# Kernel tuning notes

Hardware: AMD Instinct MI355X
Metric: run time of the kernel (lower is better)

The kernel has to match this reference:

```python
import jax, jax.numpy as jnp
import numpy as np

B, T, H = 2, 2048, 1024
NH = 16
HD = H // NH


def setup_inputs() -> dict:
    key = jax.random.key(0)
    ks = jax.random.split(key, 9)
    s = 0.02
    return {
        "x": jax.random.normal(ks[0], (B, T, H), dtype=jnp.float32),
        "attn_mask": jnp.ones((B, T), dtype=jnp.int32),
        "Wq": jax.random.normal(ks[1], (H, H), dtype=jnp.float32) * s,
        "bq": jnp.zeros((H,), dtype=jnp.float32),
        "Wk": jax.random.normal(ks[2], (H, H), dtype=jnp.float32) * s,
        "bk": jnp.zeros((H,), dtype=jnp.float32),
        "Wv": jax.random.normal(ks[3], (H, H), dtype=jnp.float32) * s,
        "bv": jnp.zeros((H,), dtype=jnp.float32),
        "Wo": jax.random.normal(ks[4], (H, H), dtype=jnp.float32) * s,
        "bo": jnp.zeros((H,), dtype=jnp.float32),
    }


def reference(x, attn_mask, Wq, bq, Wk, bk, Wv, bv, Wo, bo):
    Bc, Tc, Hc = x.shape
    scale = HD ** -0.5
    # projections; torch Linear: y = x @ W.T + b (here W stored as [in,out])
    q = (x @ Wq + bq).reshape(Bc, Tc, NH, HD).transpose(0, 2, 1, 3)  # [B,NH,T,HD]
    k = (x @ Wk + bk).reshape(Bc, Tc, NH, HD).transpose(0, 2, 1, 3)
    v = (x @ Wv + bv).reshape(Bc, Tc, NH, HD).transpose(0, 2, 1, 3)
    scores = jnp.einsum('bhqd,bhkd->bhqk', q, k) * scale  # [B,NH,T,T]
    mask = attn_mask.reshape(Bc, 1, 1, Tc)
    scores = jnp.where(mask == 0, jnp.float32(-jnp.inf), scores)
    probs = jax.nn.softmax(scores, axis=-1)
    ctx = jnp.einsum('bhqk,bhkd->bhqd', probs, v)  # [B,NH,T,HD]
    ctx = ctx.transpose(0, 2, 1, 3).reshape(Bc, Tc, Hc)
    out = ctx @ Wo + bo
    return out
```

## Files before the change

### kernel.cpp

```cpp
#include <hip/hip_runtime.h>

typedef _Float16 f16;
typedef _Float16 f16x8 __attribute__((ext_vector_type(8)));
typedef _Float16 f16x4 __attribute__((ext_vector_type(4)));
typedef __fp16 h16x2 __attribute__((ext_vector_type(2)));
typedef float f32x4 __attribute__((ext_vector_type(4)));

#define MFMA32(a, b, c) __builtin_amdgcn_mfma_f32_16x16x32_f16((a), (b), (c), 0, 0, 0)

static constexpr int Bb = 2, T = 2048, H = 1024, NH = 16, HD = 64;
static constexpr int M = Bb * T;
static constexpr int NQK = 2 * H;
#define QSCALE 0.1803368801111f

__device__ __forceinline__ void gload_lds16(const void* g, void* l) {
  __builtin_amdgcn_global_load_lds(
      (const __attribute__((address_space(1))) void*)g,
      (__attribute__((address_space(3))) void*)l, 16, 0, 0);
}

__global__ __launch_bounds__(256) void pack_all(const float* __restrict__ x,
                                                const float* __restrict__ Wq,
                                                const float* __restrict__ Wk,
                                                const float* __restrict__ Wv,
                                                const float* __restrict__ Wo,
                                                const float* __restrict__ bq,
                                                const float* __restrict__ bk,
                                                const float* __restrict__ bv,
                                                const int* __restrict__ mask,
                                                f16* __restrict__ xh,
                                                f16* __restrict__ WqkvT,
                                                f16* __restrict__ WoT,
                                                float* __restrict__ bqkv,
                                                float* __restrict__ maskf) {
  __shared__ f16 tile[64][65];
  const int bid = blockIdx.x;
  if (bid < 4096) {
    int i = bid * 256 + threadIdx.x;
    float4 v = ((const float4*)x)[i];
    f16x4 o;
    o[0] = (f16)v.x; o[1] = (f16)v.y; o[2] = (f16)v.z; o[3] = (f16)v.w;
    *(f16x4*)(xh + (size_t)i * 4) = o;
  } else if (bid < 5120) {
    int t = bid - 4096;
    int z = t >> 8, rem = t & 255;
    const float* W = (z == 0) ? Wq : (z == 1) ? Wk : (z == 2) ? Wv : Wo;
    f16* Wt = (z < 3) ? (WqkvT + (size_t)z * H * H) : WoT;
    const float scale = (z == 0) ? QSCALE : 1.0f;
    int k0 = (rem >> 4) * 64, n0 = (rem & 15) * 64;
    for (int p = 0; p < 16; ++p) {
      int idx = threadIdx.x + p * 256;
      int r = idx >> 6, c = idx & 63;
      tile[r][c] = (f16)(W[(size_t)(k0 + r) * H + n0 + c] * scale);
    }
    __syncthreads();
    for (int p = 0; p < 16; ++p) {
      int idx = threadIdx.x + p * 256;
      int r = idx >> 6, c = idx & 63;
      Wt[(size_t)(n0 + r) * H + k0 + c] = tile[c][r];
    }
  } else if (bid < 5132) {
    int i = (bid - 5120) * 256 + threadIdx.x;
    if (i < 3072) {
      float v = (i < 1024) ? bq[i] * QSCALE : ((i < 2048) ? bk[i - 1024] : bv[i - 2048]);
      bqkv[i] = v;
    }
  } else {
    int i = (bid - 5132) * 256 + threadIdx.x;
    if (i < Bb * T) maskf[i] = mask[i] ? 0.0f : -30000.0f;
  }
}

__device__ __forceinline__ f16x8 lds_frag(const f16* base, int row, int gr) {
  return *(const f16x8*)(base + row * 64 + ((gr ^ (row & 7)) << 3));
}

__global__ __launch_bounds__(256, 3) void gemm_qkv(const f16* __restrict__ A,
                                                   const f16* __restrict__ Bt,
                                                   const float* __restrict__ bias,
                                                   f16* __restrict__ QK,
                                                   f16* __restrict__ VT) {
  constexpr int TM = 128, TN = 64, Kk = 1024;
  __shared__ f16 As[2][TM * 64];
  __shared__ f16 Bs[2][TN * 64];
  const int tid = threadIdx.x;
  const int lane = tid & 63, w = tid >> 6;
  const int quad = lane >> 4, l16 = lane & 15;
  const int wm = w >> 1, wn = w & 1;
  const int m0 = blockIdx.y * TM, n0 = blockIdx.x * TN;

  f32x4 acc[4][2];
  for (int a = 0; a < 4; ++a)
    for (int b2 = 0; b2 < 2; ++b2)
      for (int r = 0; r < 4; ++r) acc[a][b2][r] = 0.f;

  auto stage = [&](int k0, int buf) {
    for (int p = 0; p < 4; ++p) {
      int slot = p * 256 + w * 64 + lane;
      int r = slot >> 3, g = (slot & 7) ^ (r & 7);
      gload_lds16(A + (size_t)(m0 + r) * Kk + k0 + g * 8,
                  (char*)&As[buf][0] + (p * 256 + w * 64) * 16);
    }
    for (int p = 0; p < 2; ++p) {
      int slot = p * 256 + w * 64 + lane;
      int r = slot >> 3, g = (slot & 7) ^ (r & 7);
      gload_lds16(Bt + (size_t)(n0 + r) * Kk + k0 + g * 8,
                  (char*)&Bs[buf][0] + (p * 256 + w * 64) * 16);
    }
  };

  stage(0, 0);
  __syncthreads();
  for (int it = 0; it < Kk / 64; ++it) {
    const int cur = it & 1;
    if (it + 1 < Kk / 64) stage((it + 1) * 64, cur ^ 1);
    for (int ks = 0; ks < 2; ++ks) {
      f16x8 af[4], bf[2];
      for (int t = 0; t < 4; ++t)
        af[t] = lds_frag(&As[cur][0], wm * 64 + t * 16 + l16, ks * 4 + quad);
      for (int t = 0; t < 2; ++t)
        bf[t] = lds_frag(&Bs[cur][0], wn * 32 + t * 16 + l16, ks * 4 + quad);
      for (int tm = 0; tm < 4; ++tm)
        for (int tn = 0; tn < 2; ++tn)
          acc[tm][tn] = MFMA32(af[tm], bf[tn], acc[tm][tn]);
    }
    __syncthreads();
  }

  if (n0 < 2048) {
    for (int tm = 0; tm < 4; ++tm)
      for (int tn = 0; tn < 2; ++tn) {
        int n = n0 + wn * 32 + tn * 16 + l16;
        float bn = bias[n];
        for (int r = 0; r < 4; ++r) {
          int m = m0 + wm * 64 + tm * 16 + quad * 4 + r;
          QK[(size_t)m * NQK + n] = (f16)(acc[tm][tn][r] + bn);
        }
      }
  } else {
    for (int tm = 0; tm < 4; ++tm)
      for (int tn = 0; tn < 2; ++tn) {
        int ng = n0 + wn * 32 + tn * 16 + l16;
        float bn = bias[ng];
        int n = ng - 2048;
        int h = n >> 6, d = n & 63;
        int mrow = m0 + wm * 64 + tm * 16 + quad * 4;
        int bb = mrow >> 11, t = mrow & 2047;
        int c = (t & ~127) | ((t + 8 * (d & 15)) & 127);
        f16x4 o;
        for (int r = 0; r < 4; ++r) o[r] = (f16)(acc[tm][tn][r] + bn);
        *(f16x4*)(VT + ((size_t)(bb * NH + h) * HD + d) * T + c) = o;
      }
  }
}

__global__ __launch_bounds__(256, 3) void gemm_out(const f16* __restrict__ A,
                                                   const f16* __restrict__ Bt,
                                                   const float* __restrict__ bias,
                                                   float* __restrict__ Cout) {
  constexpr int TM = 128, TN = 64, Kk = 1024, Nn = 1024;
  __shared__ f16 As[2][TM * 64];
  __shared__ f16 Bs[2][TN * 64];
  const int tid = threadIdx.x;
  const int lane = tid & 63, w = tid >> 6;
  const int quad = lane >> 4, l16 = lane & 15;
  const int wm = w >> 1, wn = w & 1;
  const int m0 = blockIdx.y * TM, n0 = blockIdx.x * TN;

  f32x4 acc[4][2];
  for (int a = 0; a < 4; ++a)
    for (int b2 = 0; b2 < 2; ++b2)
      for (int r = 0; r < 4; ++r) acc[a][b2][r] = 0.f;

  auto stage = [&](int k0, int buf) {
    for (int p = 0; p < 4; ++p) {
      int slot = p * 256 + w * 64 + lane;
      int r = slot >> 3, g = (slot & 7) ^ (r & 7);
      gload_lds16(A + (size_t)(m0 + r) * Kk + k0 + g * 8,
                  (char*)&As[buf][0] + (p * 256 + w * 64) * 16);
    }
    for (int p = 0; p < 2; ++p) {
      int slot = p * 256 + w * 64 + lane;
      int r = slot >> 3, g = (slot & 7) ^ (r & 7);
      gload_lds16(Bt + (size_t)(n0 + r) * Kk + k0 + g * 8,
                  (char*)&Bs[buf][0] + (p * 256 + w * 64) * 16);
    }
  };

  stage(0, 0);
  __syncthreads();
  for (int it = 0; it < Kk / 64; ++it) {
    const int cur = it & 1;
    if (it + 1 < Kk / 64) stage((it + 1) * 64, cur ^ 1);
    for (int ks = 0; ks < 2; ++ks) {
      f16x8 af[4], bf[2];
      for (int t = 0; t < 4; ++t)
        af[t] = lds_frag(&As[cur][0], wm * 64 + t * 16 + l16, ks * 4 + quad);
      for (int t = 0; t < 2; ++t)
        bf[t] = lds_frag(&Bs[cur][0], wn * 32 + t * 16 + l16, ks * 4 + quad);
      for (int tm = 0; tm < 4; ++tm)
        for (int tn = 0; tn < 2; ++tn)
          acc[tm][tn] = MFMA32(af[tm], bf[tn], acc[tm][tn]);
    }
    __syncthreads();
  }

  for (int tm = 0; tm < 4; ++tm)
    for (int tn = 0; tn < 2; ++tn) {
      int n = n0 + wn * 32 + tn * 16 + l16;
      float bn = bias[n];
      for (int r = 0; r < 4; ++r) {
        int m = m0 + wm * 64 + tm * 16 + quad * 4 + r;
        Cout[(size_t)m * Nn + n] = acc[tm][tn][r] + bn;
      }
    }
}


static constexpr int KT_ELE = 128 * 64;
static constexpr int VT_ELE = 64 * 128;

__global__ __launch_bounds__(512, 2) void attn_fused(const f16* __restrict__ QK,
                                                     const f16* __restrict__ VT,
                                                     const float* __restrict__ maskf,
                                                     f16* __restrict__ ctx) {
  __shared__ __align__(16) char smem[70656];
  f16* KtB = (f16*)smem;
  f16* VtB = (f16*)(smem + 2 * KT_ELE * 2);

  const int tid = threadIdx.x;
  const int w = tid >> 6, lane = tid & 63;
  const int quad = lane >> 4, l16 = lane & 15;
  const int qw = w & 3, g = w >> 2;

  const int flat = blockIdx.x + (T / 256) * (blockIdx.y + NH * blockIdx.z);
  const int xcd = flat & 7, idx = flat >> 3;
  const int bh = xcd * 4 + (idx >> 3);
  const int qb = idx & 7;
  const int h = bh & 15, b = bh >> 4;
  const int q0 = qb * 256;

  const size_t kbase = (size_t)(b * T) * NQK + H + h * HD;
  const size_t vtbase = ((size_t)(b * NH + h) * HD) * T;
  const float* maskp = maskf + b * T;

  f16x8 qf[4][2];
  for (int tq = 0; tq < 4; ++tq) {
    const f16* qrow = QK + (size_t)(b * T + q0 + qw * 64 + tq * 16 + l16) * NQK + h * HD;
    qf[tq][0] = *(const f16x8*)(qrow + quad * 8);
    qf[tq][1] = *(const f16x8*)(qrow + 32 + quad * 8);
  }

  f16x8 onesf;
  for (int i = 0; i < 8; ++i) onesf[i] = (f16)1.0f;

  f32x4 oacc[4][4];
  f32x4 lacc[4];
  for (int tq = 0; tq < 4; ++tq) {
    for (int r = 0; r < 4; ++r) lacc[tq][r] = 0.f;
    for (int t = 0; t < 4; ++t)
      for (int r = 0; r < 4; ++r) oacc[tq][t][r] = 0.f;
  }

  auto stage = [&](int kv0, int buf) {
    f16* Kd = KtB + buf * KT_ELE;
    f16* Vd = VtB + buf * VT_ELE;
    for (int p = 0; p < 2; ++p) {
      int s = p * 512 + tid;
      int R = s >> 3, sg = (s & 7) ^ (R & 7);
      int kv = (R & ~31) | ((R & 12) << 1) | ((R & 16) >> 2) | (R & 3);
      gload_lds16(QK + kbase + (size_t)(kv0 + kv) * NQK + sg * 8,
                  (char*)Kd + (p * 512 + w * 64) * 16);
    }
    for (int p = 0; p < 2; ++p) {
      int s = p * 512 + tid;
      int d = s >> 4, cg = s & 15;
      gload_lds16(VT + vtbase + (size_t)d * T + kv0 + cg * 8,
                  (char*)Vd + (p * 512 + w * 64) * 16);
    }
  };

  stage(0, 0);
  __syncthreads();

  for (int it = 0; it < T / 128; ++it) {
    const int cur = it & 1;
    if (it + 1 < T / 128) stage((it + 1) * 128, cur ^ 1);

    const f16* Kc = KtB + cur * KT_ELE;
    const f16* Vc = VtB + cur * VT_ELE;

    for (int s = 0; s < 2; ++s) {
      const int bi = g * 2 + s;
      const int kvabs = it * 128 + bi * 32;
      float4 m0 = *(const float4*)(maskp + kvabs + quad * 8);
      float4 m1 = *(const float4*)(maskp + kvabs + quad * 8 + 4);
      f32x4 zA, zB;
      zA[0] = m0.x; zA[1] = m0.y; zA[2] = m0.z; zA[3] = m0.w;
      zB[0] = m1.x; zB[1] = m1.y; zB[2] = m1.z; zB[3] = m1.w;
      f16x8 kfA0 = lds_frag(Kc, bi * 32 + l16, quad);
      f16x8 kfA1 = lds_frag(Kc, bi * 32 + l16, 4 + quad);
      f16x8 kfB0 = lds_frag(Kc, bi * 32 + 16 + l16, quad);
      f16x8 kfB1 = lds_frag(Kc, bi * 32 + 16 + l16, 4 + quad);
      f16x8 vf[4];
      for (int td = 0; td < 4; ++td)
        vf[td] = *(const f16x8*)&Vc[(td * 16 + l16) * 128 +
                                    ((bi * 32 + quad * 8 + 8 * l16) & 127)];

      f32x4 sA[4], sB[4];
      for (int tq = 0; tq < 4; ++tq) {
        sA[tq] = MFMA32(kfA0, qf[tq][0], zA);
        sB[tq] = MFMA32(kfB0, qf[tq][0], zB);
      }
      for (int tq = 0; tq < 4; ++tq) {
        sA[tq] = MFMA32(kfA1, qf[tq][1], sA[tq]);
        sB[tq] = MFMA32(kfB1, qf[tq][1], sB[tq]);
      }

      f16x8 pf[4];
      for (int tq = 0; tq < 4; ++tq) {
        float pA0 = __builtin_amdgcn_exp2f(sA[tq][0]);
        float pA1 = __builtin_amdgcn_exp2f(sA[tq][1]);
        float pA2 = __builtin_amdgcn_exp2f(sA[tq][2]);
        float pA3 = __builtin_amdgcn_exp2f(sA[tq][3]);
        float pB0 = __builtin_amdgcn_exp2f(sB[tq][0]);
        float pB1 = __builtin_amdgcn_exp2f(sB[tq][1]);
        float pB2 = __builtin_amdgcn_exp2f(sB[tq][2]);
        float pB3 = __builtin_amdgcn_exp2f(sB[tq][3]);
        union PF { f16x8 v; h16x2 h[4]; } u;
        u.h[0] = __builtin_amdgcn_cvt_pkrtz(pA0, pA1);
        u.h[1] = __builtin_amdgcn_cvt_pkrtz(pA2, pA3);
        u.h[2] = __builtin_amdgcn_cvt_pkrtz(pB0, pB1);
        u.h[3] = __builtin_amdgcn_cvt_pkrtz(pB2, pB3);
        pf[tq] = u.v;
      }

      for (int tq = 0; tq < 4; ++tq) {
        for (int td = 0; td < 4; ++td)
          oacc[tq][td] = MFMA32(vf[td], pf[tq], oacc[tq][td]);
        lacc[tq] = MFMA32(onesf, pf[tq], lacc[tq]);
      }
    }
    __syncthreads();
  }

  float* cmb = (float*)smem;
  const int slot = qw * 64 + lane;
  if (g == 1) {
    float* dst = cmb + slot * 69;
    int i = 0;
    for (int tq = 0; tq < 4; ++tq)
      for (int td = 0; td < 4; ++td)
        for (int r = 0; r < 4; ++r) dst[i++] = oacc[tq][td][r];
    for (int tq = 0; tq < 4; ++tq) dst[64 + tq] = lacc[tq][0];
  }
  __syncthreads();
  if (g == 0) {
    const float* src = cmb + slot * 69;
    int i = 0;
    for (int tq = 0; tq < 4; ++tq)
      for (int td = 0; td < 4; ++td)
        for (int r = 0; r < 4; ++r) oacc[tq][td][r] += src[i++];

    for (int tq = 0; tq < 4; ++tq) {
      float l = lacc[tq][0] + src[64 + tq];
      float inv = 1.f / l;
      int row = b * T + q0 + qw * 64 + tq * 16 + l16;
      for (int td = 0; td < 4; ++td) {
        f16x4 o;
        for (int r = 0; r < 4; ++r) o[r] = (f16)(oacc[tq][td][r] * inv);
        *(f16x4*)(ctx + (size_t)row * H + h * HD + td * 16 + quad * 4) = o;
      }
    }
  }
}


extern "C" void kernel_launch(void* const* d_in, const int* in_sizes, int n_in,
                              void* d_out, int out_size, void* d_ws, size_t ws_size,
                              hipStream_t stream) {
  const float* x  = (const float*)d_in[0];
  const int* mask = (const int*)d_in[1];
  const float* Wq = (const float*)d_in[2];
  const float* bq = (const float*)d_in[3];
  const float* Wk = (const float*)d_in[4];
  const float* bk = (const float*)d_in[5];
  const float* Wv = (const float*)d_in[6];
  const float* bv = (const float*)d_in[7];
  const float* Wo = (const float*)d_in[8];
  const float* bo = (const float*)d_in[9];
  float* out = (float*)d_out;

  char* ws = (char*)d_ws;
  f16* xh      = (f16*)(ws);
  f16* Wqkv_t  = (f16*)(ws + (8u  << 20));
  f16* Wot     = (f16*)(ws + (14u << 20));
  float* bqkv  = (float*)(ws + (16u << 20));
  float* maskf = (float*)(ws + (16u << 20) + 65536);
  f16* QK      = (f16*)(ws + (17u << 20));
  f16* ctx     = (f16*)(ws + (34u << 20));
  f16* VTr     = (f16*)(ws + (43u << 20));

  pack_all<<<dim3(5164), 256, 0, stream>>>(x, Wq, Wk, Wv, Wo, bq, bk, bv, mask,
                                           xh, Wqkv_t, Wot, bqkv, maskf);

  gemm_qkv<<<dim3(3 * H / 64, M / 128), 256, 0, stream>>>(
      xh, Wqkv_t, bqkv, QK, VTr);

  attn_fused<<<dim3(T / 256, NH, Bb), 512, 0, stream>>>(QK, VTr, maskf, ctx);

  gemm_out<<<dim3(H / 64, M / 128), 256, 0, stream>>>(ctx, Wot, bo, out);
}
```

Before: 184.6 us.

## Rewrite QKV GEMM as 256x256 tiled, phased-barrier pipeline with XCD-aware block remap

The QKV projection GEMM moves from 128x64 tiles with 256 threads to 256x256 tiles with 512 threads. Each wave accumulates a 128x64 sub-tile, and the main loop is hand-scheduled into phases that interleave LDS fragment loads, MFMA quads at raised priority, and half-tile global-to-LDS staging, separated by sched barriers and explicit vmcnt waits. Both the QKV and output GEMMs remap block indices so neighbouring tiles land on the same XCD to improve L2 reuse. The goals are higher arithmetic intensity per LDS byte and better overlap of memory with MFMA. The costs are only 192 blocks for the QKV GEMM, which may leave some CUs idle, heavy register use, and 128KB of LDS per block.

```diff
diff --git a/kernel.cpp b/kernel.cpp
--- a/kernel.cpp
+++ b/kernel.cpp
@@ -18,6 +18,12 @@
       (const __attribute__((address_space(1))) void*)g,
       (__attribute__((address_space(3))) void*)l, 16, 0, 0);
 }
+
+#define PHASE_BAR()                         \
+  do {                                      \
+    __builtin_amdgcn_sched_barrier(0);      \
+    __builtin_amdgcn_s_barrier();           \
+  } while (0)
 
 __global__ __launch_bounds__(256) void pack_all(const float* __restrict__ x,
                                                 const float* __restrict__ Wq,
@@ -75,76 +81,169 @@
   return *(const f16x8*)(base + row * 64 + ((gr ^ (row & 7)) << 3));
 }
 
-__global__ __launch_bounds__(256, 3) void gemm_qkv(const f16* __restrict__ A,
-                                                   const f16* __restrict__ Bt,
-                                                   const float* __restrict__ bias,
-                                                   f16* __restrict__ QK,
-                                                   f16* __restrict__ VT) {
-  constexpr int TM = 128, TN = 64, Kk = 1024;
-  __shared__ f16 As[2][TM * 64];
-  __shared__ f16 Bs[2][TN * 64];
+__global__ __launch_bounds__(512) void gemm_qkv(const f16* __restrict__ A,
+                                                const f16* __restrict__ Bt,
+                                                const float* __restrict__ bias,
+                                                f16* __restrict__ QK,
+                                                f16* __restrict__ VT) {
+  constexpr int Kk = 1024;
+  __shared__ f16 lds[2][2][256 * 64];
   const int tid = threadIdx.x;
   const int lane = tid & 63, w = tid >> 6;
   const int quad = lane >> 4, l16 = lane & 15;
-  const int wm = w >> 1, wn = w & 1;
-  const int m0 = blockIdx.y * TM, n0 = blockIdx.x * TN;
-
-  f32x4 acc[4][2];
-  for (int a = 0; a < 4; ++a)
-    for (int b2 = 0; b2 < 2; ++b2)
+  const int wm = w >> 2, wn = w & 3;
+
+  const int flat = blockIdx.y * 12 + blockIdx.x;
+  const int xcd = flat & 7, li = flat >> 3;
+  const int bx = (xcd & 1) * 6 + li % 6;
+  const int by = (xcd >> 1) * 4 + li / 6;
+  const int m0 = by * 256, n0 = bx * 256;
+
+  f32x4 acc[8][4];
+#pragma unroll
+  for (int a = 0; a < 8; ++a)
+#pragma unroll
+    for (int b2 = 0; b2 < 4; ++b2)
       for (int r = 0; r < 4; ++r) acc[a][b2][r] = 0.f;
 
-  auto stage = [&](int k0, int buf) {
-    for (int p = 0; p < 4; ++p) {
-      int slot = p * 256 + w * 64 + lane;
-      int r = slot >> 3, g = (slot & 7) ^ (r & 7);
-      gload_lds16(A + (size_t)(m0 + r) * Kk + k0 + g * 8,
-                  (char*)&As[buf][0] + (p * 256 + w * 64) * 16);
-    }
-    for (int p = 0; p < 2; ++p) {
-      int slot = p * 256 + w * 64 + lane;
-      int r = slot >> 3, g = (slot & 7) ^ (r & 7);
-      gload_lds16(Bt + (size_t)(n0 + r) * Kk + k0 + g * 8,
-                  (char*)&Bs[buf][0] + (p * 256 + w * 64) * 16);
-    }
-  };
-
-  stage(0, 0);
-  __syncthreads();
-  for (int it = 0; it < Kk / 64; ++it) {
-    const int cur = it & 1;
-    if (it + 1 < Kk / 64) stage((it + 1) * 64, cur ^ 1);
-    for (int ks = 0; ks < 2; ++ks) {
-      f16x8 af[4], bf[2];
-      for (int t = 0; t < 4; ++t)
-        af[t] = lds_frag(&As[cur][0], wm * 64 + t * 16 + l16, ks * 4 + quad);
-      for (int t = 0; t < 2; ++t)
-        bf[t] = lds_frag(&Bs[cur][0], wn * 32 + t * 16 + l16, ks * 4 + quad);
-      for (int tm = 0; tm < 4; ++tm)
-        for (int tn = 0; tn < 2; ++tn)
-          acc[tm][tn] = MFMA32(af[tm], bf[tn], acc[tm][tn]);
-    }
-    __syncthreads();
+  auto stageA = [&](int kt, int buf, int oddbit) {
+#pragma unroll
+    for (int j = 0; j < 2; ++j) {
+      int s = j * 512 + tid;
+      int rr = s >> 3, gs = s & 7;
+      int r = ((rr & 64) << 1) | oddbit | (rr & 63);
+      int g = gs ^ (r & 7);
+      int rr0 = j * 64 + w * 8;
+      int r0 = ((rr0 & 64) << 1) | oddbit | (rr0 & 63);
+      gload_lds16(A + (size_t)(m0 + r) * Kk + kt * 64 + g * 8,
+                  (char*)&lds[buf][0][0] + r0 * 128);
+    }
+  };
+  auto stageB = [&](int kt, int buf, int oddbit) {
+#pragma unroll
+    for (int j = 0; j < 2; ++j) {
+      int s = j * 512 + tid;
+      int rr = s >> 3, gs = s & 7;
+      int r = ((rr & 96) << 1) | oddbit | (rr & 31);
+      int g = gs ^ (r & 7);
+      int rr0 = j * 64 + w * 8;
+      int r0 = ((rr0 & 96) << 1) | oddbit | (rr0 & 31);
+      gload_lds16(Bt + (size_t)(n0 + r) * Kk + kt * 64 + g * 8,
+                  (char*)&lds[buf][1][0] + r0 * 128);
+    }
+  };
+
+  f16x8 afr[4][2], bfr0[2][2], bfr1[2][2];
+
+  auto loadA = [&](const f16* Ab, int tmh) {
+#pragma unroll
+    for (int t4 = 0; t4 < 4; ++t4)
+#pragma unroll
+      for (int kk = 0; kk < 2; ++kk)
+        afr[t4][kk] = lds_frag(Ab, wm * 128 + tmh * 64 + t4 * 16 + l16, kk * 4 + quad);
+  };
+  auto loadB = [&](const f16* Bbp, int tnh, f16x8 (*dst)[2]) {
+#pragma unroll
+    for (int t2 = 0; t2 < 2; ++t2)
+#pragma unroll
+      for (int kk = 0; kk < 2; ++kk)
+        dst[t2][kk] = lds_frag(Bbp, wn * 64 + tnh * 32 + t2 * 16 + l16, kk * 4 + quad);
+  };
+  auto quadMfma = [&](f16x8 (*bf)[2], int tmh, int tnh) {
+    __builtin_amdgcn_s_setprio(1);
+#pragma unroll
+    for (int kk = 0; kk < 2; ++kk)
+#pragma unroll
+      for (int t4 = 0; t4 < 4; ++t4)
+#pragma unroll
+        for (int t2 = 0; t2 < 2; ++t2)
+          acc[tmh * 4 + t4][tnh * 2 + t2] =
+              MFMA32(afr[t4][kk], bf[t2][kk], acc[tmh * 4 + t4][tnh * 2 + t2]);
+    __builtin_amdgcn_s_setprio(0);
+  };
+
+  const f16* A0 = &lds[0][0][0];
+  const f16* B0l = &lds[0][1][0];
+  const f16* A1 = &lds[1][0][0];
+  const f16* B1l = &lds[1][1][0];
+
+  stageA(0, 0, 0); stageB(0, 0, 0); stageA(0, 0, 64); stageB(0, 0, 32);
+  stageA(1, 1, 0); stageB(1, 1, 0); stageA(1, 1, 64); stageB(1, 1, 32);
+  asm volatile("s_waitcnt vmcnt(8)" ::: "memory");
+  PHASE_BAR();
+
+  for (int i = 0; i < 8; ++i) {
+    const bool more = (i < 7);
+    const int ta = 2 * i + 2, tb = 2 * i + 3;
+
+    loadA(A0, 0);
+    loadB(B0l, 0, bfr0);
+    PHASE_BAR();
+    quadMfma(bfr0, 0, 0);
+    PHASE_BAR();
+    if (more) { stageA(ta, 0, 0); stageB(ta, 0, 0); }
+    loadB(B0l, 1, bfr1);
+    PHASE_BAR();
+    quadMfma(bfr1, 0, 1);
+    PHASE_BAR();
+    if (more) stageB(ta, 0, 32);
+    loadA(A0, 1);
+    PHASE_BAR();
+    quadMfma(bfr1, 1, 1);
+    PHASE_BAR();
+    if (more) stageA(ta, 0, 64);
+    PHASE_BAR();
+    quadMfma(bfr0, 1, 0);
+    if (more) asm volatile("s_waitcnt vmcnt(8)" ::: "memory");
+    else      asm volatile("s_waitcnt vmcnt(0)" ::: "memory");
+    PHASE_BAR();
+
+    loadA(A1, 0);
+    loadB(B1l, 0, bfr0);
+    PHASE_BAR();
+    quadMfma(bfr0, 0, 0);
+    PHASE_BAR();
+    if (more) { stageA(tb, 1, 0); stageB(tb, 1, 0); }
+    loadB(B1l, 1, bfr1);
+    PHASE_BAR();
+    quadMfma(bfr1, 0, 1);
+    PHASE_BAR();
+    if (more) stageB(tb, 1, 32);
+    loadA(A1, 1);
+    PHASE_BAR();
+    quadMfma(bfr1, 1, 1);
+    PHASE_BAR();
+    if (more) stageA(tb, 1, 64);
+    PHASE_BAR();
+    quadMfma(bfr0, 1, 0);
+    if (more) {
+      asm volatile("s_waitcnt vmcnt(8)" ::: "memory");
+      PHASE_BAR();
+    }
   }
 
   if (n0 < 2048) {
-    for (int tm = 0; tm < 4; ++tm)
-      for (int tn = 0; tn < 2; ++tn) {
-        int n = n0 + wn * 32 + tn * 16 + l16;
+#pragma unroll
+    for (int tm = 0; tm < 8; ++tm)
+#pragma unroll
+      for (int tn = 0; tn < 4; ++tn) {
+        int n = n0 + wn * 64 + tn * 16 + l16;
         float bn = bias[n];
         for (int r = 0; r < 4; ++r) {
-          int m = m0 + wm * 64 + tm * 16 + quad * 4 + r;
+          int m = m0 + wm * 128 + tm * 16 + quad * 4 + r;
           QK[(size_t)m * NQK + n] = (f16)(acc[tm][tn][r] + bn);
         }
       }
   } else {
-    for (int tm = 0; tm < 4; ++tm)
-      for (int tn = 0; tn < 2; ++tn) {
-        int ng = n0 + wn * 32 + tn * 16 + l16;
+#pragma unroll
+    for (int tm = 0; tm < 8; ++tm)
+#pragma unroll
+      for (int tn = 0; tn < 4; ++tn) {
+        int ng = n0 + wn * 64 + tn * 16 + l16;
         float bn = bias[ng];
         int n = ng - 2048;
         int h = n >> 6, d = n & 63;
-        int mrow = m0 + wm * 64 + tm * 16 + quad * 4;
+        int mrow = m0 + wm * 128 + tm * 16 + quad * 4;
         int bb = mrow >> 11, t = mrow & 2047;
         int c = (t & ~127) | ((t + 8 * (d & 15)) & 127);
         f16x4 o;
@@ -165,7 +264,12 @@
   const int lane = tid & 63, w = tid >> 6;
   const int quad = lane >> 4, l16 = lane & 15;
   const int wm = w >> 1, wn = w & 1;
-  const int m0 = blockIdx.y * TM, n0 = blockIdx.x * TN;
+
+  const int flat = blockIdx.y * 16 + blockIdx.x;
+  const int xq = flat & 7, xr = flat >> 3;
+  const int bx = (xq & 1) * 8 + (xr % 8);
+  const int by = (xq >> 1) * 8 + (xr / 8);
+  const int m0 = by * TM, n0 = bx * TN;
 
   f32x4 acc[4][2];
   for (int a = 0; a < 4; ++a)
@@ -404,8 +508,7 @@
   pack_all<<<dim3(5164), 256, 0, stream>>>(x, Wq, Wk, Wv, Wo, bq, bk, bv, mask,
                                            xh, Wqkv_t, Wot, bqkv, maskf);
 
-  gemm_qkv<<<dim3(3 * H / 64, M / 128), 256, 0, stream>>>(
-      xh, Wqkv_t, bqkv, QK, VTr);
+  gemm_qkv<<<dim3(12, 16), 512, 0, stream>>>(xh, Wqkv_t, bqkv, QK, VTr);
 
   attn_fused<<<dim3(T / 256, NH, Bb), 512, 0, stream>>>(QK, VTr, maskf, ctx);
 
```

Result: slower. 196.5 us (+6.5%).

## Fuse attention and output projection into one persistent kernel with grid barrier

Applied to the files above, without the earlier changes.

Merges the attention kernel and the output-projection GEMM into a single 256-block launch. A global atomic counter acts as a grid-wide barrier between the two phases, and the GEMM phase switches to 128x128 tiles with 512 threads. This removes one kernel launch and its gap, at the cost of an extra memset and a spin barrier that needs all 256 blocks to be co-resident. It also lowers GEMM parallelism from 512 blocks of 256 threads to 256 blocks.

```diff
diff --git a/kernel.cpp b/kernel.cpp
--- a/kernel.cpp
+++ b/kernel.cpp
@@ -154,76 +154,18 @@
   }
 }
 
-__global__ __launch_bounds__(256, 3) void gemm_out(const f16* __restrict__ A,
-                                                   const f16* __restrict__ Bt,
-                                                   const float* __restrict__ bias,
-                                                   float* __restrict__ Cout) {
-  constexpr int TM = 128, TN = 64, Kk = 1024, Nn = 1024;
-  __shared__ f16 As[2][TM * 64];
-  __shared__ f16 Bs[2][TN * 64];
-  const int tid = threadIdx.x;
-  const int lane = tid & 63, w = tid >> 6;
-  const int quad = lane >> 4, l16 = lane & 15;
-  const int wm = w >> 1, wn = w & 1;
-  const int m0 = blockIdx.y * TM, n0 = blockIdx.x * TN;
-
-  f32x4 acc[4][2];
-  for (int a = 0; a < 4; ++a)
-    for (int b2 = 0; b2 < 2; ++b2)
-      for (int r = 0; r < 4; ++r) acc[a][b2][r] = 0.f;
-
-  auto stage = [&](int k0, int buf) {
-    for (int p = 0; p < 4; ++p) {
-      int slot = p * 256 + w * 64 + lane;
-      int r = slot >> 3, g = (slot & 7) ^ (r & 7);
-      gload_lds16(A + (size_t)(m0 + r) * Kk + k0 + g * 8,
-                  (char*)&As[buf][0] + (p * 256 + w * 64) * 16);
-    }
-    for (int p = 0; p < 2; ++p) {
-      int slot = p * 256 + w * 64 + lane;
-      int r = slot >> 3, g = (slot & 7) ^ (r & 7);
-      gload_lds16(Bt + (size_t)(n0 + r) * Kk + k0 + g * 8,
-                  (char*)&Bs[buf][0] + (p * 256 + w * 64) * 16);
-    }
-  };
-
-  stage(0, 0);
-  __syncthreads();
-  for (int it = 0; it < Kk / 64; ++it) {
-    const int cur = it & 1;
-    if (it + 1 < Kk / 64) stage((it + 1) * 64, cur ^ 1);
-    for (int ks = 0; ks < 2; ++ks) {
-      f16x8 af[4], bf[2];
-      for (int t = 0; t < 4; ++t)
-        af[t] = lds_frag(&As[cur][0], wm * 64 + t * 16 + l16, ks * 4 + quad);
-      for (int t = 0; t < 2; ++t)
-        bf[t] = lds_frag(&Bs[cur][0], wn * 32 + t * 16 + l16, ks * 4 + quad);
-      for (int tm = 0; tm < 4; ++tm)
-        for (int tn = 0; tn < 2; ++tn)
-          acc[tm][tn] = MFMA32(af[tm], bf[tn], acc[tm][tn]);
-    }
-    __syncthreads();
-  }
-
-  for (int tm = 0; tm < 4; ++tm)
-    for (int tn = 0; tn < 2; ++tn) {
-      int n = n0 + wn * 32 + tn * 16 + l16;
-      float bn = bias[n];
-      for (int r = 0; r < 4; ++r) {
-        int m = m0 + wm * 64 + tm * 16 + quad * 4 + r;
-        Cout[(size_t)m * Nn + n] = acc[tm][tn][r] + bn;
-      }
-    }
-}
-
 
 static constexpr int KT_ELE = 128 * 64;
 static constexpr int VT_ELE = 64 * 128;
 
-__global__ __launch_bounds__(512, 2) void attn_fused(const f16* __restrict__ QK,
-                                                     const f16* __restrict__ VT,
-                                                     const float* __restrict__ maskf,
-                                                     f16* __restrict__ ctx) {
+__global__ __launch_bounds__(512, 2) void attn_out(const f16* __restrict__ QK,
+                                                   const f16* __restrict__ VT,
+                                                   const float* __restrict__ maskf,
+                                                   f16* __restrict__ ctx,
+                                                   const f16* __restrict__ WoT,
+                                                   const float* __restrict__ bo,
+                                                   float* __restrict__ out,
+                                                   unsigned* __restrict__ gctr) {
   __shared__ __align__(16) char smem[70656];
   f16* KtB = (f16*)smem;
   f16* VtB = (f16*)(smem + 2 * KT_ELE * 2);
@@ -233,145 +175,213 @@
   const int quad = lane >> 4, l16 = lane & 15;
   const int qw = w & 3, g = w >> 2;
 
-  const int flat = blockIdx.x + (T / 256) * (blockIdx.y + NH * blockIdx.z);
-  const int xcd = flat & 7, idx = flat >> 3;
-  const int bh = xcd * 4 + (idx >> 3);
-  const int qb = idx & 7;
-  const int h = bh & 15, b = bh >> 4;
-  const int q0 = qb * 256;
-
-  const size_t kbase = (size_t)(b * T) * NQK + H + h * HD;
-  const size_t vtbase = ((size_t)(b * NH + h) * HD) * T;
-  const float* maskp = maskf + b * T;
-
-  f16x8 qf[4][2];
-  for (int tq = 0; tq < 4; ++tq) {
-    const f16* qrow = QK + (size_t)(b * T + q0 + qw * 64 + tq * 16 + l16) * NQK + h * HD;
-    qf[tq][0] = *(const f16x8*)(qrow + quad * 8);
-    qf[tq][1] = *(const f16x8*)(qrow + 32 + quad * 8);
-  }
-
-  f16x8 onesf;
-  for (int i = 0; i < 8; ++i) onesf[i] = (f16)1.0f;
-
-  f32x4 oacc[4][4];
-  f32x4 lacc[4];
-  for (int tq = 0; tq < 4; ++tq) {
-    for (int r = 0; r < 4; ++r) lacc[tq][r] = 0.f;
-    for (int t = 0; t < 4; ++t)
-      for (int r = 0; r < 4; ++r) oacc[tq][t][r] = 0.f;
-  }
-
-  auto stage = [&](int kv0, int buf) {
-    f16* Kd = KtB + buf * KT_ELE;
-    f16* Vd = VtB + buf * VT_ELE;
-    for (int p = 0; p < 2; ++p) {
-      int s = p * 512 + tid;
-      int R = s >> 3, sg = (s & 7) ^ (R & 7);
-      int kv = (R & ~31) | ((R & 12) << 1) | ((R & 16) >> 2) | (R & 3);
-      gload_lds16(QK + kbase + (size_t)(kv0 + kv) * NQK + sg * 8,
-                  (char*)Kd + (p * 512 + w * 64) * 16);
-    }
-    for (int p = 0; p < 2; ++p) {
-      int s = p * 512 + tid;
-      int d = s >> 4, cg = s & 15;
-      gload_lds16(VT + vtbase + (size_t)d * T + kv0 + cg * 8,
-                  (char*)Vd + (p * 512 + w * 64) * 16);
-    }
-  };
-
-  stage(0, 0);
+  {
+    const int flat = blockIdx.x;
+    const int xcd = flat & 7, idx = flat >> 3;
+    const int bh = xcd * 4 + (idx >> 3);
+    const int qb = idx & 7;
+    const int h = bh & 15, b = bh >> 4;
+    const int q0 = qb * 256;
+
+    const size_t kbase = (size_t)(b * T) * NQK + H + h * HD;
+    const size_t vtbase = ((size_t)(b * NH + h) * HD) * T;
+    const float* maskp = maskf + b * T;
+
+    f16x8 qf[4][2];
+    for (int tq = 0; tq < 4; ++tq) {
+      const f16* qrow = QK + (size_t)(b * T + q0 + qw * 64 + tq * 16 + l16) * NQK + h * HD;
+      qf[tq][0] = *(const f16x8*)(qrow + quad * 8);
+      qf[tq][1] = *(const f16x8*)(qrow + 32 + quad * 8);
+    }
+
+    f16x8 onesf;
+    for (int i = 0; i < 8; ++i) onesf[i] = (f16)1.0f;
+
+    f32x4 oacc[4][4];
+    f32x4 lacc[4];
+    for (int tq = 0; tq < 4; ++tq) {
+      for (int r = 0; r < 4; ++r) lacc[tq][r] = 0.f;
+      for (int t = 0; t < 4; ++t)
+        for (int r = 0; r < 4; ++r) oacc[tq][t][r] = 0.f;
+    }
+
+    auto stage = [&](int kv0, int buf) {
+      f16* Kd = KtB + buf * KT_ELE;
+      f16* Vd = VtB + buf * VT_ELE;
+      for (int p = 0; p < 2; ++p) {
+        int s = p * 512 + tid;
+        int R = s >> 3, sg = (s & 7) ^ (R & 7);
+        int kv = (R & ~31) | ((R & 12) << 1) | ((R & 16) >> 2) | (R & 3);
+        gload_lds16(QK + kbase + (size_t)(kv0 + kv) * NQK + sg * 8,
+                    (char*)Kd + (p * 512 + w * 64) * 16);
+      }
+      for (int p = 0; p < 2; ++p) {
+        int s = p * 512 + tid;
+        int d = s >> 4, cg = s & 15;
+        gload_lds16(VT + vtbase + (size_t)d * T + kv0 + cg * 8,
+                    (char*)Vd + (p * 512 + w * 64) * 16);
+      }
+    };
+
+    stage(0, 0);
+    __syncthreads();
+
+    for (int it = 0; it < T / 128; ++it) {
+      const int cur = it & 1;
+      if (it + 1 < T / 128) stage((it + 1) * 128, cur ^ 1);
+
+      const f16* Kc = KtB + cur * KT_ELE;
+      const f16* Vc = VtB + cur * VT_ELE;
+
+      for (int s = 0; s < 2; ++s) {
+        const int bi = g * 2 + s;
+        const int kvabs = it * 128 + bi * 32;
+        float4 m0 = *(const float4*)(maskp + kvabs + quad * 8);
+        float4 m1 = *(const float4*)(maskp + kvabs + quad * 8 + 4);
+        f32x4 zA, zB;
+        zA[0] = m0.x; zA[1] = m0.y; zA[2] = m0.z; zA[3] = m0.w;
+        zB[0] = m1.x; zB[1] = m1.y; zB[2] = m1.z; zB[3] = m1.w;
+        f16x8 kfA0 = lds_frag(Kc, bi * 32 + l16, quad);
+        f16x8 kfA1 = lds_frag(Kc, bi * 32 + l16, 4 + quad);
+        f16x8 kfB0 = lds_frag(Kc, bi * 32 + 16 + l16, quad);
+        f16x8 kfB1 = lds_frag(Kc, bi * 32 + 16 + l16, 4 + quad);
+        f16x8 vf[4];
+        for (int td = 0; td < 4; ++td)
+          vf[td] = *(const f16x8*)&Vc[(td * 16 + l16) * 128 +
+                                      ((bi * 32 + quad * 8 + 8 * l16) & 127)];
+
+        f32x4 sA[4], sB[4];
+        for (int tq = 0; tq < 4; ++tq) {
+          sA[tq] = MFMA32(kfA0, qf[tq][0], zA);
+          sB[tq] = MFMA32(kfB0, qf[tq][0], zB);
+        }
+        for (int tq = 0; tq < 4; ++tq) {
+          sA[tq] = MFMA32(kfA1, qf[tq][1], sA[tq]);
+          sB[tq] = MFMA32(kfB1, qf[tq][1], sB[tq]);
+        }
+
+        f16x8 pf[4];
+        for (int tq = 0; tq < 4; ++tq) {
+          float pA0 = __builtin_amdgcn_exp2f(sA[tq][0]);
+          float pA1 = __builtin_amdgcn_exp2f(sA[tq][1]);
+          float pA2 = __builtin_amdgcn_exp2f(sA[tq][2]);
+          float pA3 = __builtin_amdgcn_exp2f(sA[tq][3]);
+          float pB0 = __builtin_amdgcn_exp2f(sB[tq][0]);
+          float pB1 = __builtin_amdgcn_exp2f(sB[tq][1]);
+          float pB2 = __builtin_amdgcn_exp2f(sB[tq][2]);
+          float pB3 = __builtin_amdgcn_exp2f(sB[tq][3]);
+          union PF { f16x8 v; h16x2 h[4]; } u;
+          u.h[0] = __builtin_amdgcn_cvt_pkrtz(pA0, pA1);
+          u.h[1] = __builtin_amdgcn_cvt_pkrtz(pA2, pA3);
+          u.h[2] = __builtin_amdgcn_cvt_pkrtz(pB0, pB1);
+          u.h[3] = __builtin_amdgcn_cvt_pkrtz(pB2, pB3);
+          pf[tq] = u.v;
+        }
+
+        for (int tq = 0; tq < 4; ++tq) {
+          for (int td = 0; td < 4; ++td)
+            oacc[tq][td] = MFMA32(vf[td], pf[tq], oacc[tq][td]);
+          lacc[tq] = MFMA32(onesf, pf[tq], lacc[tq]);
+        }
+      }
+      __syncthreads();
+    }
+
+    float* cmb = (float*)smem;
+    const int slot = qw * 64 + lane;
+    if (g == 1) {
+      float* dst = cmb + slot * 69;
+      int i = 0;
+      for (int tq = 0; tq < 4; ++tq)
+        for (int td = 0; td < 4; ++td)
+          for (int r = 0; r < 4; ++r) dst[i++] = oacc[tq][td][r];
+      for (int tq = 0; tq < 4; ++tq) dst[64 + tq] = lacc[tq][0];
+    }
+    __syncthreads();
+    if (g == 0) {
+      const float* src = cmb + slot * 69;
+      int i = 0;
+      for (int tq = 0; tq < 4; ++tq)
+        for (int td = 0; td < 4; ++td)
+          for (int r = 0; r < 4; ++r) oacc[tq][td][r] += src[i++];
+
+      for (int tq = 0; tq < 4; ++tq) {
+        float l = lacc[tq][0] + src[64 + tq];
+        float inv = 1.f / l;
+        int row = b * T + q0 + qw * 64 + tq * 16 + l16;
+        for (int td = 0; td < 4; ++td) {
+          f16x4 o;
+          for (int r = 0; r < 4; ++r) o[r] = (f16)(oacc[tq][td][r] * inv);
+          *(f16x4*)(ctx + (size_t)row * H + h * HD + td * 16 + quad * 4) = o;
+        }
+      }
+    }
+  }
+
   __syncthreads();
-
-  for (int it = 0; it < T / 128; ++it) {
-    const int cur = it & 1;
-    if (it + 1 < T / 128) stage((it + 1) * 128, cur ^ 1);
-
-    const f16* Kc = KtB + cur * KT_ELE;
-    const f16* Vc = VtB + cur * VT_ELE;
-
-    for (int s = 0; s < 2; ++s) {
-      const int bi = g * 2 + s;
-      const int kvabs = it * 128 + bi * 32;
-      float4 m0 = *(const float4*)(maskp + kvabs + quad * 8);
-      float4 m1 = *(const float4*)(maskp + kvabs + quad * 8 + 4);
-      f32x4 zA, zB;
-      zA[0] = m0.x; zA[1] = m0.y; zA[2] = m0.z; zA[3] = m0.w;
-      zB[0] = m1.x; zB[1] = m1.y; zB[2] = m1.z; zB[3] = m1.w;
-      f16x8 kfA0 = lds_frag(Kc, bi * 32 + l16, quad);
-      f16x8 kfA1 = lds_frag(Kc, bi * 32 + l16, 4 + quad);
-      f16x8 kfB0 = lds_frag(Kc, bi * 32 + 16 + l16, quad);
-      f16x8 kfB1 = lds_frag(Kc, bi * 32 + 16 + l16, 4 + quad);
-      f16x8 vf[4];
-      for (int td = 0; td < 4; ++td)
-        vf[td] = *(const f16x8*)&Vc[(td * 16 + l16) * 128 +
-                                    ((bi * 32 + quad * 8 + 8 * l16) & 127)];
-
-      f32x4 sA[4], sB[4];
-      for (int tq = 0; tq < 4; ++tq) {
-        sA[tq] = MFMA32(kfA0, qf[tq][0], zA);
-        sB[tq] = MFMA32(kfB0, qf[tq][0], zB);
-      }
-      for (int tq = 0; tq < 4; ++tq) {
-        sA[tq] = MFMA32(kfA1, qf[tq][1], sA[tq]);
-        sB[tq] = MFMA32(kfB1, qf[tq][1], sB[tq]);
-      }
-
-      f16x8 pf[4];
-      for (int tq = 0; tq < 4; ++tq) {
-        float pA0 = __builtin_amdgcn_exp2f(sA[tq][0]);
-        float pA1 = __builtin_amdgcn_exp2f(sA[tq][1]);
-        float pA2 = __builtin_amdgcn_exp2f(sA[tq][2]);
-        float pA3 = __builtin_amdgcn_exp2f(sA[tq][3]);
-        float pB0 = __builtin_amdgcn_exp2f(sB[tq][0]);
-        float pB1 = __builtin_amdgcn_exp2f(sB[tq][1]);
-        float pB2 = __builtin_amdgcn_exp2f(sB[tq][2]);
-        float pB3 = __builtin_amdgcn_exp2f(sB[tq][3]);
-        union PF { f16x8 v; h16x2 h[4]; } u;
-        u.h[0] = __builtin_amdgcn_cvt_pkrtz(pA0, pA1);
-        u.h[1] = __builtin_amdgcn_cvt_pkrtz(pA2, pA3);
-        u.h[2] = __builtin_amdgcn_cvt_pkrtz(pB0, pB1);
-        u.h[3] = __builtin_amdgcn_cvt_pkrtz(pB2, pB3);
-        pf[tq] = u.v;
-      }
-
-      for (int tq = 0; tq < 4; ++tq) {
-        for (int td = 0; td < 4; ++td)
-          oacc[tq][td] = MFMA32(vf[td], pf[tq], oacc[tq][td]);
-        lacc[tq] = MFMA32(onesf, pf[tq], lacc[tq]);
-      }
-    }
+  if (tid == 0) {
+    __threadfence();
+    atomicAdd(gctr, 1u);
+    while (atomicAdd(gctr, 0u) < 256u) { }
+  }
+  __syncthreads();
+  __threadfence();
+
+  {
+    constexpr int Kk = 1024, Nn = 1024;
+    f16* As = (f16*)smem;
+    f16* Bs = (f16*)(smem + 32768);
+    const int wm = w >> 2, wn = w & 3;
+    const int gid = blockIdx.x;
+    const int m0 = (gid >> 3) * 128, n0 = (gid & 7) * 128;
+
+    f32x4 acc[4][2];
+    for (int a = 0; a < 4; ++a)
+      for (int b2 = 0; b2 < 2; ++b2)
+        for (int r = 0; r < 4; ++r) acc[a][b2][r] = 0.f;
+
+    auto stage2 = [&](int k0, int buf) {
+      for (int p = 0; p < 2; ++p) {
+        int slot = p * 512 + tid;
+        int r = slot >> 3, gg = (slot & 7) ^ (r & 7);
+        gload_lds16(ctx + (size_t)(m0 + r) * Kk + k0 + gg * 8,
+                    (char*)As + buf * 16384 + (p * 512 + w * 64) * 16);
+      }
+      for (int p = 0; p < 2; ++p) {
+        int slot = p * 512 + tid;
+        int r = slot >> 3, gg = (slot & 7) ^ (r & 7);
+        gload_lds16(WoT + (size_t)(n0 + r) * Kk + k0 + gg * 8,
+                    (char*)Bs + buf * 16384 + (p * 512 + w * 64) * 16);
+      }
+    };
+
+    stage2(0, 0);
     __syncthreads();
-  }
-
-  float* cmb = (float*)smem;
-  const int slot = qw * 64 + lane;
-  if (g == 1) {
-    float* dst = cmb + slot * 69;
-    int i = 0;
-    for (int tq = 0; tq < 4; ++tq)
-      for (int td = 0; td < 4; ++td)
-        for (int r = 0; r < 4; ++r) dst[i++] = oacc[tq][td][r];
-    for (int tq = 0; tq < 4; ++tq) dst[64 + tq] = lacc[tq][0];
-  }
-  __syncthreads();
-  if (g == 0) {
-    const float* src = cmb + slot * 69;
-    int i = 0;
-    for (int tq = 0; tq < 4; ++tq)
-      for (int td = 0; td < 4; ++td)
-        for (int r = 0; r < 4; ++r) oacc[tq][td][r] += src[i++];
-
-    for (int tq = 0; tq < 4; ++tq) {
-      float l = lacc[tq][0] + src[64 + tq];
-      float inv = 1.f / l;
-      int row = b * T + q0 + qw * 64 + tq * 16 + l16;
-      for (int td = 0; td < 4; ++td) {
-        f16x4 o;
-        for (int r = 0; r < 4; ++r) o[r] = (f16)(oacc[tq][td][r] * inv);
-        *(f16x4*)(ctx + (size_t)row * H + h * HD + td * 16 + quad * 4) = o;
-      }
-    }
+    for (int it = 0; it < Kk / 64; ++it) {
+      const int cur = it & 1;
+      if (it + 1 < Kk / 64) stage2((it + 1) * 64, cur ^ 1);
+      for (int ks = 0; ks < 2; ++ks) {
+        f16x8 af[4], bf[2];
+        for (int t = 0; t < 4; ++t)
+          af[t] = lds_frag(As + cur * 8192, wm * 64 + t * 16 + l16, ks * 4 + quad);
+        for (int t = 0; t < 2; ++t)
+          bf[t] = lds_frag(Bs + cur * 8192, wn * 32 + t * 16 + l16, ks * 4 + quad);
+        for (int tm = 0; tm < 4; ++tm)
+          for (int tn = 0; tn < 2; ++tn)
+            acc[tm][tn] = MFMA32(af[tm], bf[tn], acc[tm][tn]);
+      }
+      __syncthreads();
+    }
+
+    for (int tm = 0; tm < 4; ++tm)
+      for (int tn = 0; tn < 2; ++tn) {
+        int n = n0 + wn * 32 + tn * 16 + l16;
+        float bn = bo[n];
+        for (int r = 0; r < 4; ++r) {
+          int m = m0 + wm * 64 + tm * 16 + quad * 4 + r;
+          out[(size_t)m * Nn + n] = acc[tm][tn][r] + bn;
+        }
+      }
   }
 }
 
@@ -400,6 +410,9 @@
   f16* QK      = (f16*)(ws + (17u << 20));
   f16* ctx     = (f16*)(ws + (34u << 20));
   f16* VTr     = (f16*)(ws + (43u << 20));
+  unsigned* gctr = (unsigned*)(ws + (51u << 20));
+
+  hipMemsetAsync(gctr, 0, sizeof(unsigned), stream);
 
   pack_all<<<dim3(5164), 256, 0, stream>>>(x, Wq, Wk, Wv, Wo, bq, bk, bv, mask,
                                            xh, Wqkv_t, Wot, bqkv, maskf);
@@ -407,7 +420,6 @@
   gemm_qkv<<<dim3(3 * H / 64, M / 128), 256, 0, stream>>>(
       xh, Wqkv_t, bqkv, QK, VTr);
 
-  attn_fused<<<dim3(T / 256, NH, Bb), 512, 0, stream>>>(QK, VTr, maskf, ctx);
-
-  gemm_out<<<dim3(H / 64, M / 128), 256, 0, stream>>>(ctx, Wot, bo, out);
-}
+  attn_out<<<dim3(256), 512, 0, stream>>>(QK, VTr, maskf, ctx, Wot, bo, out,
+                                          gctr);
+}
```

Result: slower. 229.1 us (+24.1%).
